# Optimization experiments

Measured on AMD Instinct MI355X. Metric: run time of the kernel, lower is better.

Reference implementation:

```python
import jax, jax.numpy as jnp
import numpy as np
from jax import lax

R = 4                      # search_range
FILTERS = [128, 128, 96, 64, 32, 2]
B, H, W, C = 8, 128, 128, 128
IN_CH = (2 * R + 1) ** 2 + C + 2   # 81 + 128 + 2 = 211


def mish(x):
    return x * jnp.tanh(jax.nn.softplus(x))


def sepconv(x, dw, pw, b=None, act=True):
    # depthwise 3x3 (SAME) then pointwise 1x1, matching SeparableConv2D
    cin = x.shape[-1]
    y = lax.conv_general_dilated(
        x, dw, window_strides=(1, 1), padding='SAME',
        dimension_numbers=('NHWC', 'HWIO', 'NHWC'),
        feature_group_count=cin)
    y = jnp.einsum('bhwc,co->bhwo', y, pw)
    if b is not None:
        y = y + b
    return mish(y) if act else y


def warp(img, flo):
    # bilinear backward warp; TF casts float->int32 with truncation, jnp matches
    b_, h, w, _ = img.shape
    xs = jnp.arange(w, dtype=jnp.float32)[None, None, :]
    ys = jnp.arange(h, dtype=jnp.float32)[None, :, None]
    x = xs + flo[..., 0]
    y = ys + flo[..., 1]
    x0 = x.astype(jnp.int32)
    y0 = y.astype(jnp.int32)
    x1 = x0 + 1
    y1 = y0 + 1
    x0c = jnp.clip(x0, 0, w - 1)
    x1c = jnp.clip(x1, 0, w - 1)
    y0c = jnp.clip(y0, 0, h - 1)
    y1c = jnp.clip(y1, 0, h - 1)
    bi = jnp.arange(b_)[:, None, None]
    Ia = img[bi, y0c, x0c]
    Ib = img[bi, y1c, x0c]
    Ic = img[bi, y0c, x1c]
    Id = img[bi, y1c, x1c]
    x0f = x0c.astype(jnp.float32); x1f = x1c.astype(jnp.float32)
    y0f = y0c.astype(jnp.float32); y1f = y1c.astype(jnp.float32)
    wa = ((x1f - x) * (y1f - y))[..., None]
    wb = ((x1f - x) * (y - y0f))[..., None]
    wc = ((x - x0f) * (y1f - y))[..., None]
    wd = ((x - x0f) * (y - y0f))[..., None]
    return wa * Ia + wb * Ib + wc * Ic + wd * Id


def cost_volume(prv, nxt):
    _, h, w, _ = prv.shape
    d = 2 * R + 1
    pad = jnp.pad(nxt, ((0, 0), (R, R), (R, R), (0, 0)))
    costs = [jnp.mean(prv * pad[:, i:i + h, j:j + w, :], axis=-1)
             for i in range(d) for j in range(d)]
    return jnp.stack(costs, axis=-1)  # [B,H,W,81]


def setup_inputs() -> dict:
    key = jax.random.key(0)
    ks = iter(jax.random.split(key, 64))
    inp = {
        'prv': jax.random.normal(next(ks), (B, H, W, C), dtype=jnp.float32),
        'nxt': jax.random.normal(next(ks), (B, H, W, C), dtype=jnp.float32),
        'flo': jax.random.normal(next(ks), (B, H, W, 2), dtype=jnp.float32),
    }
    cin = IN_CH
    for i, f in enumerate(FILTERS):
        inp[f'dw{i}'] = 0.05 * jax.random.normal(next(ks), (3, 3, 1, cin), dtype=jnp.float32)
        inp[f'pw{i}'] = 0.05 * jax.random.normal(next(ks), (cin, f), dtype=jnp.float32)
        if i < len(FILTERS) - 1:
            inp[f'b{i}'] = 0.05 * jax.random.normal(next(ks), (f,), dtype=jnp.float32)
        cin = f
    return inp


def reference(prv, nxt, flo,
              dw0, pw0, b0, dw1, pw1, b1, dw2, pw2, b2,
              dw3, pw3, b3, dw4, pw4, b4, dw5, pw5):
    nxt_w = warp(nxt, flo)
    cost = cost_volume(prv, nxt_w)
    x = jnp.concatenate([cost, prv, flo], axis=-1)  # [B,H,W,211]
    x = sepconv(x, dw0, pw0, b0)
    x = sepconv(x, dw1, pw1, b1)
    x = sepconv(x, dw2, pw2, b2)
    x = sepconv(x, dw3, pw3, b3)
    x = sepconv(x, dw4, pw4, b4)
    x = sepconv(x, dw5, pw5, None, act=False)  # final flow, no bias/activation
    return x
```

## Files before the change

kernel.cpp:

```cpp
#include <hip/hip_runtime.h>
#include <hip/hip_bf16.h>

#define B_ 8
#define H_ 128
#define W_ 128
#define C_ 128

using f32x4 = __attribute__((ext_vector_type(4))) float;
using s16x8 = __attribute__((ext_vector_type(8))) short;
using us4   = __attribute__((ext_vector_type(4))) unsigned short;

__device__ __forceinline__ float mish_f(float x) {
    float t = __expf(fminf(x, 20.0f));
    float u = t * (t + 2.0f);
    return x * u / (u + 2.0f);
}

__device__ __forceinline__ int swz_row(int blk) {
    return ((blk & 7) << 7) | (blk >> 3);
}

__device__ __forceinline__ unsigned short f2bf_rne(float x) {
    unsigned u = __builtin_bit_cast(unsigned, x);
    u += 0x7FFFu + ((u >> 16) & 1u);
    return (unsigned short)(u >> 16);
}
__device__ __forceinline__ float bf2f(unsigned short h) {
    unsigned u = ((unsigned)h) << 16;
    return __builtin_bit_cast(float, u);
}
__device__ __forceinline__ unsigned short f2bf_hw(float x) {
    return __bfloat16_as_ushort(__float2bfloat16(x));
}

__device__ __forceinline__ f32x4 load4u(const float* p) {
    f32x4 v;
    __builtin_memcpy(&v, p, 16);
    return v;
}

__global__ __launch_bounds__(256) void warp_kernel(
    const float* __restrict__ nxt, const float* __restrict__ flo,
    unsigned short* __restrict__ nwh, unsigned short* __restrict__ nwl)
{
    const int tid = threadIdx.x;
    const int c   = tid & 127;
    const int pix = blockIdx.x * 2 + (tid >> 7);
    const int b   = pix >> 14;
    const int rem = pix & 16383;
    const int y   = rem >> 7;
    const int x   = rem & 127;

    const float fx = flo[(size_t)pix * 2 + 0];
    const float fy = flo[(size_t)pix * 2 + 1];
    const float xf = (float)x + fx;
    const float yf = (float)y + fy;
    const int x0 = (int)xf;
    const int y0 = (int)yf;
    const int x0c = min(max(x0, 0), W_ - 1);
    const int x1c = min(max(x0 + 1, 0), W_ - 1);
    const int y0c = min(max(y0, 0), H_ - 1);
    const int y1c = min(max(y0 + 1, 0), H_ - 1);
    const float x0f = (float)x0c, x1f = (float)x1c;
    const float y0f = (float)y0c, y1f = (float)y1c;
    const float wa = (x1f - xf) * (y1f - yf);
    const float wb = (x1f - xf) * (yf - y0f);
    const float wc = (xf - x0f) * (y1f - yf);
    const float wd = (xf - x0f) * (yf - y0f);

    const float* base = nxt + (size_t)b * H_ * W_ * C_;
    const float Ia = base[((size_t)y0c * W_ + x0c) * C_ + c];
    const float Ib = base[((size_t)y1c * W_ + x0c) * C_ + c];
    const float Ic = base[((size_t)y0c * W_ + x1c) * C_ + c];
    const float Id = base[((size_t)y1c * W_ + x1c) * C_ + c];
    const float v  = wa * Ia + wb * Ib + wc * Ic + wd * Id;

    const unsigned short h = f2bf_hw(v);
    const unsigned short l = f2bf_hw(v - bf2f(h));
    nwh[(size_t)pix * C_ + c] = h;
    nwl[(size_t)pix * C_ + c] = l;
}

__global__ __launch_bounds__(1024, 4) void costvol_mfma_kernel(
    const float* __restrict__ prv,
    const unsigned short* __restrict__ nwh,
    const unsigned short* __restrict__ nwl,
    float* __restrict__ cost)
{
    __shared__ float scr[8][576];

    const int tid  = threadIdx.x;
    const int lane = tid & 63;
    const int wv   = tid >> 6;
    const int w    = wv >> 1;
    const int nt   = wv & 1;
    const int r    = swz_row(blockIdx.x);
    const int y    = r & 127;
    const int b    = r >> 7;
    const int m15  = lane & 15;
    const int ko   = (lane >> 4) * 8;

    const int  xs   = (w + nt) * 16 + m15 - 8;
    const bool xok  = (xs >= 0) && (xs < W_);
    const int  xoff = (xok ? xs : 0) * C_ + ko;

    f32x4 acc[9];
    #pragma unroll
    for (int d = 0; d < 9; ++d) acc[d] = (f32x4){0.f, 0.f, 0.f, 0.f};

    const float* pbase = prv + ((size_t)r * W_ + (w * 16 + m15)) * C_ + ko;

    for (int kt = 0; kt < 4; ++kt) {
        const f32x4 p0 = *(const f32x4*)(pbase + kt * 32);
        const f32x4 p1 = *(const f32x4*)(pbase + kt * 32 + 4);
        s16x8 ahi, alo;
        #pragma unroll
        for (int j = 0; j < 8; ++j) {
            const float f = (j < 4) ? p0[j] : p1[j - 4];
            const unsigned short hh = f2bf_hw(f);
            ahi[j] = (short)hh;
            alo[j] = (short)f2bf_hw(f - bf2f(hh));
        }

        const size_t kb = (size_t)kt * 32 + xoff;
        #pragma unroll
        for (int d = 0; d < 9; ++d) {
            const int q = y + d - 4;
            if (q >= 0 && q < H_) {
                const size_t off = ((size_t)(b * H_ + q) * W_) * C_ + kb;
                s16x8 bhi = (s16x8){0,0,0,0,0,0,0,0};
                s16x8 blo = (s16x8){0,0,0,0,0,0,0,0};
                if (xok) {
                    bhi = *(const s16x8*)(nwh + off);
                    blo = *(const s16x8*)(nwl + off);
                }
                acc[d] = __builtin_amdgcn_mfma_f32_16x16x32_bf16(alo, bhi, acc[d], 0, 0, 0);
                acc[d] = __builtin_amdgcn_mfma_f32_16x16x32_bf16(ahi, blo, acc[d], 0, 0, 0);
                acc[d] = __builtin_amdgcn_mfma_f32_16x16x32_bf16(ahi, bhi, acc[d], 0, 0, 0);
            }
        }
    }

    const int quad = lane >> 4;
    #pragma unroll
    for (int d = 0; d < 9; ++d) {
        __syncthreads();
        #pragma unroll
        for (int g = 0; g < 4; ++g)
            scr[w][(quad * 4 + g) * 36 + nt * 16 + m15] = acc[d][g];
        __syncthreads();
        #pragma unroll
        for (int p = 0; p < 2; ++p) {
            const int local = lane + 64 * p;
            if (local < 72) {
                const int idx = nt * 72 + local;
                const int xl  = idx / 9;
                const int dx  = idx - xl * 9;
                const float v = scr[w][xl * 37 + dx + 4] * (1.0f / 128.0f);
                cost[((size_t)r * W_ + (w * 16 + xl)) * 81 + d * 9 + dx] = v;
            }
        }
    }
}

__global__ __launch_bounds__(256) void prep_kernel(
    const float* __restrict__ pw, int CIN, int COUT, int NT,
    unsigned short* __restrict__ hi, unsigned short* __restrict__ lo)
{
    const int kt = blockIdx.x / NT;
    const int nt = blockIdx.x - kt * NT;
    #pragma unroll
    for (int s = 0; s < 2; ++s) {
        const int e = threadIdx.x + 256 * s;
        const int n = e >> 5, k = e & 31;
        const int kg = kt * 32 + k, ng = nt * 16 + n;
        const float v = (kg < CIN && ng < COUT) ? pw[(size_t)kg * COUT + ng] : 0.0f;
        const unsigned short h = f2bf_rne(v);
        const unsigned short l = f2bf_rne(v - bf2f(h));
        const size_t o = ((size_t)blockIdx.x * 16 + n) * 32 + k;
        hi[o] = h; lo[o] = l;
    }
}

template<int CIN, int COUT, bool ACT, bool IS_L0>
__global__ __launch_bounds__(512, 4) void sepconv_kernel(
    const float* __restrict__ in,
    const float* __restrict__ cost, const float* __restrict__ prv,
    const float* __restrict__ flo,
    const float* __restrict__ dw,
    const unsigned short* __restrict__ Bhi, const unsigned short* __restrict__ Blo,
    const float* __restrict__ bias, float* __restrict__ out)
{
    constexpr int KT   = (CIN + 31) / 32;
    constexpr int KPAD = KT * 32;
    constexpr int NT   = (COUT + 15) / 16;
    constexpr int KSTR = 40;
    __shared__ unsigned short Ahi[128 * KSTR];
    __shared__ unsigned short Alo[128 * KSTR];
    __shared__ float dwl[9 * KPAD];

    const int tid  = threadIdx.x;
    const int lane = tid & 63;
    const int w    = tid >> 6;
    const int r    = swz_row(blockIdx.x);
    const int h    = r & 127;
    const int b    = r >> 7;

    const int co = (tid & 7) * 4;
    const int xb = (tid >> 3) * 2;

    bool rowok[3]; int rowpix[3];
    #pragma unroll
    for (int ky = 0; ky < 3; ++ky) {
        const int yy = h + ky - 1;
        rowok[ky]  = (yy >= 0) && (yy < H_);
        rowpix[ky] = (b * H_ + (rowok[ky] ? yy : h)) * W_;
    }

    for (int i = tid; i < 9 * KPAD; i += 512) {
        const int t = i / KPAD, c = i - t * KPAD;
        dwl[i] = (c < CIN) ? dw[t * CIN + c] : 0.0f;
    }

    f32x4 acc[NT];
    #pragma unroll
    for (int n = 0; n < NT; ++n)
        acc[n] = (f32x4){0.0f, 0.0f, 0.0f, 0.0f};

    __syncthreads();

    for (int kt = 0; kt < KT; ++kt) {
        const int cg = kt * 32 + co;
        f32x4 V[3][4];
        #pragma unroll
        for (int ky = 0; ky < 3; ++ky) {
            #pragma unroll
            for (int xm = 0; xm < 4; ++xm) {
                const int xx = xb - 1 + xm;
                f32x4 v = (f32x4){0.f, 0.f, 0.f, 0.f};
                if (rowok[ky] && xx >= 0 && xx < W_) {
                    const int px = rowpix[ky] + xx;
                    if constexpr (IS_L0) {
                        if (cg <= 76) {
                            v = load4u(cost + (size_t)px * 81 + cg);
                        } else if (cg == 80) {
                            const float* cp = cost + (size_t)px * 81;
                            const float* pp = prv + (size_t)px * 128;
                            v = (f32x4){cp[80], pp[0], pp[1], pp[2]};
                        } else if (cg <= 204) {
                            v = load4u(prv + (size_t)px * 128 + (cg - 81));
                        } else if (cg == 208) {
                            const float* pp = prv + (size_t)px * 128;
                            const float* fp = flo + (size_t)px * 2;
                            v = (f32x4){pp[127], fp[0], fp[1], 0.f};
                        }
                    } else {
                        v = *(const f32x4*)(in + (size_t)px * CIN + cg);
                    }
                }
                V[ky][xm] = v;
            }
        }

        f32x4 a0 = (f32x4){0.f, 0.f, 0.f, 0.f};
        f32x4 a1 = (f32x4){0.f, 0.f, 0.f, 0.f};
        #pragma unroll
        for (int ky = 0; ky < 3; ++ky) {
            #pragma unroll
            for (int kx = 0; kx < 3; ++kx) {
                const f32x4 wv = *(const f32x4*)&dwl[(ky * 3 + kx) * KPAD + cg];
                a0 += wv * V[ky][kx];
                a1 += wv * V[ky][kx + 1];
            }
        }

        us4 h0, l0, h1, l1;
        #pragma unroll
        for (int j = 0; j < 4; ++j) {
            const unsigned short hh0 = f2bf_hw(a0[j]);
            h0[j] = hh0; l0[j] = f2bf_hw(a0[j] - bf2f(hh0));
            const unsigned short hh1 = f2bf_hw(a1[j]);
            h1[j] = hh1; l1[j] = f2bf_hw(a1[j] - bf2f(hh1));
        }

        __syncthreads();
        *(us4*)&Ahi[(xb + 0) * KSTR + co] = h0;
        *(us4*)&Ahi[(xb + 1) * KSTR + co] = h1;
        *(us4*)&Alo[(xb + 0) * KSTR + co] = l0;
        *(us4*)&Alo[(xb + 1) * KSTR + co] = l1;
        __syncthreads();

        const int mrow = w * 16 + (lane & 15);
        const int ko   = (lane >> 4) * 8;
        const s16x8 ahi = *(const s16x8*)&Ahi[mrow * KSTR + ko];
        const s16x8 alo = *(const s16x8*)&Alo[mrow * KSTR + ko];
        #pragma unroll
        for (int nt = 0; nt < NT; ++nt) {
            const size_t boff = (((size_t)(kt * NT + nt)) * 16 + (lane & 15)) * 32
                              + (size_t)ko;
            const s16x8 bhi = *(const s16x8*)&Bhi[boff];
            const s16x8 blo = *(const s16x8*)&Blo[boff];
            acc[nt] = __builtin_amdgcn_mfma_f32_16x16x32_bf16(alo, bhi, acc[nt], 0, 0, 0);
            acc[nt] = __builtin_amdgcn_mfma_f32_16x16x32_bf16(ahi, blo, acc[nt], 0, 0, 0);
            acc[nt] = __builtin_amdgcn_mfma_f32_16x16x32_bf16(ahi, bhi, acc[nt], 0, 0, 0);
        }
    }

    const int n    = lane & 15;
    const int quad = lane >> 4;
    #pragma unroll
    for (int nt = 0; nt < NT; ++nt) {
        const int o = nt * 16 + n;
        if ((COUT % 16 == 0) || (o < COUT)) {
            const float bv = ACT ? bias[o] : 0.0f;
            #pragma unroll
            for (int reg = 0; reg < 4; ++reg) {
                const int px = w * 16 + quad * 4 + reg;
                const float v = acc[nt][reg] + bv;
                out[((size_t)r * W_ + px) * COUT + o] = ACT ? mish_f(v) : v;
            }
        }
    }
}

extern "C" void kernel_launch(void* const* d_in, const int* in_sizes, int n_in,
                              void* d_out, int out_size, void* d_ws, size_t ws_size,
                              hipStream_t stream)
{
    (void)in_sizes; (void)n_in; (void)out_size; (void)ws_size;
    const float* prv = (const float*)d_in[0];
    const float* nxt = (const float*)d_in[1];
    const float* flo = (const float*)d_in[2];
    const float* dw0 = (const float*)d_in[3];
    const float* pw0 = (const float*)d_in[4];
    const float* b0  = (const float*)d_in[5];
    const float* dw1 = (const float*)d_in[6];
    const float* pw1 = (const float*)d_in[7];
    const float* b1  = (const float*)d_in[8];
    const float* dw2 = (const float*)d_in[9];
    const float* pw2 = (const float*)d_in[10];
    const float* b2  = (const float*)d_in[11];
    const float* dw3 = (const float*)d_in[12];
    const float* pw3 = (const float*)d_in[13];
    const float* b3  = (const float*)d_in[14];
    const float* dw4 = (const float*)d_in[15];
    const float* pw4 = (const float*)d_in[16];
    const float* b4  = (const float*)d_in[17];
    const float* dw5 = (const float*)d_in[18];
    const float* pw5 = (const float*)d_in[19];

    char* ws = (char*)d_ws;
    float* bufA = (float*)ws;
    float* bufC = (float*)(ws + 67108864);
    float* costb = bufC;
    float* l4out = (float*)(ws + 67108864 + 33554432);
    float* outp  = (float*)d_out;

    unsigned short* nwh = (unsigned short*)ws;
    unsigned short* nwl = (unsigned short*)(ws + 33554432);

    unsigned short* W0h = (unsigned short*)(ws + 112000000);
    unsigned short* W0l = (unsigned short*)(ws + 112000000 + 57344);
    unsigned short* W1h = (unsigned short*)d_out;
    unsigned short* W1l = (unsigned short*)d_out + 16384;
    unsigned short* W2h = (unsigned short*)(ws + 50331648);
    unsigned short* W2l = (unsigned short*)(ws + 50356224);
    unsigned short* W3h = (unsigned short*)(ws + 50380800);
    unsigned short* W3l = (unsigned short*)(ws + 50393088);
    unsigned short* W4h = (unsigned short*)(ws + 50405376);
    unsigned short* W4l = (unsigned short*)(ws + 50409472);
    unsigned short* W5h = (unsigned short*)(ws + 50413568);
    unsigned short* W5l = (unsigned short*)(ws + 50414592);

    const float* nullf = nullptr;

    warp_kernel<<<65536, 256, 0, stream>>>(nxt, flo, nwh, nwl);
    costvol_mfma_kernel<<<1024, 1024, 0, stream>>>(prv, nwh, nwl, costb);

    prep_kernel<<<7 * 8, 256, 0, stream>>>(pw0, 211, 128, 8, W0h, W0l);
    prep_kernel<<<4 * 8, 256, 0, stream>>>(pw1, 128, 128, 8, W1h, W1l);

    sepconv_kernel<211, 128, true,  true ><<<1024, 512, 0, stream>>>(
        nullf, costb, prv, flo, dw0, W0h, W0l, b0, bufA);
    sepconv_kernel<128, 128, true,  false><<<1024, 512, 0, stream>>>(
        bufA, nullf, nullf, nullf, dw1, W1h, W1l, b1, bufC);

    prep_kernel<<<4 * 6, 256, 0, stream>>>(pw2, 128,  96, 6, W2h, W2l);
    prep_kernel<<<3 * 4, 256, 0, stream>>>(pw3,  96,  64, 4, W3h, W3l);
    prep_kernel<<<2 * 2, 256, 0, stream>>>(pw4,  64,  32, 2, W4h, W4l);
    prep_kernel<<<1 * 1, 256, 0, stream>>>(pw5,  32,   2, 1, W5h, W5l);

    sepconv_kernel<128,  96, true,  false><<<1024, 512, 0, stream>>>(
        bufC, nullf, nullf, nullf, dw2, W2h, W2l, b2, bufA);
    sepconv_kernel< 96,  64, true,  false><<<1024, 512, 0, stream>>>(
        bufA, nullf, nullf, nullf, dw3, W3h, W3l, b3, bufC);
    sepconv_kernel< 64,  32, true,  false><<<1024, 512, 0, stream>>>(
        bufC, nullf, nullf, nullf, dw4, W4h, W4l, b4, l4out);
    sepconv_kernel< 32,   2, false, false><<<1024, 512, 0, stream>>>(
        l4out, nullf, nullf, nullf, dw5, W5h, W5l, nullf, outp);
}
```

Before: 633.5 us.

## Stage warped next-frame rows in swizzled LDS for cost-volume MFMA

The cost-volume kernel now cooperatively loads each displaced row of the warped next-frame hi/lo bf16 planes into shared memory with an XOR swizzle and zero-padded borders. MFMA B-operands are then read from LDS rather than issuing redundant global loads per wave, since the two n-tiles across waves overlap. The prv A-operands are converted to bf16 once up front and held in registers. In exchange the kernel adds about 36KB of LDS and several block-wide barriers per displacement row, and the 9 accumulators are now computed one at a time instead of interleaved.

Result: faster. 569.9 us, median of 2 (-10.0%).

```diff
diff --git a/kernel.cpp b/kernel.cpp
--- a/kernel.cpp
+++ b/kernel.cpp
@@ -87,6 +87,8 @@
     const unsigned short* __restrict__ nwl,
     float* __restrict__ cost)
 {
+    __shared__ __align__(16) unsigned short Nhi[144 * 64];
+    __shared__ __align__(16) unsigned short Nlo[144 * 64];
     __shared__ float scr[8][576];
 
     const int tid  = threadIdx.x;
@@ -98,56 +100,82 @@
     const int y    = r & 127;
     const int b    = r >> 7;
     const int m15  = lane & 15;
-    const int ko   = (lane >> 4) * 8;
-
-    const int  xs   = (w + nt) * 16 + m15 - 8;
-    const bool xok  = (xs >= 0) && (xs < W_);
-    const int  xoff = (xok ? xs : 0) * C_ + ko;
-
-    f32x4 acc[9];
+    const int kq   = lane >> 4;
+
+    const float* pbase = prv + ((size_t)r * W_ + (w * 16 + m15)) * C_ + kq * 8;
+    s16x8 ahi[4], alo[4];
     #pragma unroll
-    for (int d = 0; d < 9; ++d) acc[d] = (f32x4){0.f, 0.f, 0.f, 0.f};
-
-    const float* pbase = prv + ((size_t)r * W_ + (w * 16 + m15)) * C_ + ko;
-
     for (int kt = 0; kt < 4; ++kt) {
         const f32x4 p0 = *(const f32x4*)(pbase + kt * 32);
         const f32x4 p1 = *(const f32x4*)(pbase + kt * 32 + 4);
-        s16x8 ahi, alo;
         #pragma unroll
         for (int j = 0; j < 8; ++j) {
             const float f = (j < 4) ? p0[j] : p1[j - 4];
             const unsigned short hh = f2bf_hw(f);
-            ahi[j] = (short)hh;
-            alo[j] = (short)f2bf_hw(f - bf2f(hh));
-        }
-
-        const size_t kb = (size_t)kt * 32 + xoff;
-        #pragma unroll
-        for (int d = 0; d < 9; ++d) {
-            const int q = y + d - 4;
-            if (q >= 0 && q < H_) {
-                const size_t off = ((size_t)(b * H_ + q) * W_) * C_ + kb;
-                s16x8 bhi = (s16x8){0,0,0,0,0,0,0,0};
-                s16x8 blo = (s16x8){0,0,0,0,0,0,0,0};
-                if (xok) {
-                    bhi = *(const s16x8*)(nwh + off);
-                    blo = *(const s16x8*)(nwl + off);
+            ahi[kt][j] = (short)hh;
+            alo[kt][j] = (short)f2bf_hw(f - bf2f(hh));
+        }
+    }
+
+    {
+        const int plane = tid >> 9;
+        const int rem   = tid & 511;
+        const int side  = rem >> 8;
+        const int rem2  = rem & 255;
+        const int px    = (side ? 136 : 0) + (rem2 >> 5);
+        const int dwi   = rem2 & 31;
+        unsigned int* dst = (unsigned int*)
+            ((plane ? (char*)Nlo : (char*)Nhi) + (size_t)px * 128) + dwi;
+        *dst = 0u;
+    }
+    __syncthreads();
+
+    const int px_mem = (w + nt) * 16 + m15;
+    const int swz    = px_mem & 7;
+    const int quad   = lane >> 4;
+
+    for (int d = 0; d < 9; ++d) {
+        const int q = y + d - 4;
+        f32x4 acc = (f32x4){0.f, 0.f, 0.f, 0.f};
+
+        if (q >= 0 && q < H_) {
+            const size_t rowb = ((size_t)(b * H_ + q) * W_) * C_;
+            #pragma unroll
+            for (int kp = 0; kp < 2; ++kp) {
+                __syncthreads();
+                #pragma unroll
+                for (int s = 0; s < 2; ++s) {
+                    const int grp   = wv * 2 + s;
+                    const int plane = grp >> 4;
+                    const int ci    = (grp & 15) * 64 + lane;
+                    const int pxi   = ci >> 3;
+                    const int slot  = ci & 7;
+                    const unsigned short* src =
+                        (plane ? nwl : nwh) + rowb
+                        + (size_t)pxi * 128 + kp * 64 + slot * 8;
+                    const s16x8 v = *(const s16x8*)src;
+                    char* bse = plane ? (char*)Nlo : (char*)Nhi;
+                    *(s16x8*)(bse + (size_t)(pxi + 8) * 128
+                                  + ((slot ^ (pxi & 7)) * 16)) = v;
                 }
-                acc[d] = __builtin_amdgcn_mfma_f32_16x16x32_bf16(alo, bhi, acc[d], 0, 0, 0);
-                acc[d] = __builtin_amdgcn_mfma_f32_16x16x32_bf16(ahi, blo, acc[d], 0, 0, 0);
-                acc[d] = __builtin_amdgcn_mfma_f32_16x16x32_bf16(ahi, bhi, acc[d], 0, 0, 0);
+                __syncthreads();
+                #pragma unroll
+                for (int j = 0; j < 2; ++j) {
+                    const int kt      = kp * 2 + j;
+                    const int byteoff = px_mem * 128 + (((j * 4 + kq) ^ swz) * 16);
+                    const s16x8 bhi = *(const s16x8*)((const char*)Nhi + byteoff);
+                    const s16x8 blo = *(const s16x8*)((const char*)Nlo + byteoff);
+                    acc = __builtin_amdgcn_mfma_f32_16x16x32_bf16(alo[kt], bhi, acc, 0, 0, 0);
+                    acc = __builtin_amdgcn_mfma_f32_16x16x32_bf16(ahi[kt], blo, acc, 0, 0, 0);
+                    acc = __builtin_amdgcn_mfma_f32_16x16x32_bf16(ahi[kt], bhi, acc, 0, 0, 0);
+                }
             }
         }
-    }
-
-    const int quad = lane >> 4;
-    #pragma unroll
-    for (int d = 0; d < 9; ++d) {
+
         __syncthreads();
         #pragma unroll
         for (int g = 0; g < 4; ++g)
-            scr[w][(quad * 4 + g) * 36 + nt * 16 + m15] = acc[d][g];
+            scr[w][(quad * 4 + g) * 36 + nt * 16 + m15] = acc[g];
         __syncthreads();
         #pragma unroll
         for (int p = 0; p < 2; ++p) {
```
